# Optimization experiments

Measured on AMD Instinct MI355X. Metric: run time of the kernel, lower is better.

Reference implementation:

```python
import itertools
import jax, jax.numpy as jnp
import numpy as np

N_NODES = 100000
N_EDGES = 1600000
D = 32
C = 16
PDIM = 2  # pseudo-coordinate dim (SplineConv dim=E)


def setup_inputs() -> dict:
    key = jax.random.key(0)
    ks = jax.random.split(key, 16)
    s = 0.1
    inp = {
        "x": jax.random.normal(ks[0], (N_NODES, D), jnp.float32),
        "edge_index": jax.random.randint(ks[1], (2, N_EDGES), 0, N_NODES, jnp.int32),
        "edge_attr": jax.random.uniform(ks[2], (N_EDGES, PDIM), jnp.float32),
        # SplineConv 1: kernel_size=3 per dim -> K1 = 3**PDIM weight matrices
        "W1": jax.random.normal(ks[3], (3 ** PDIM, D, D), jnp.float32) * s,
        "root1": jax.random.normal(ks[4], (D, D), jnp.float32) * s,
        "bias1": jax.random.normal(ks[5], (D,), jnp.float32) * s,
        # SplineConv 2: kernel_size=5 per dim -> K2 = 5**PDIM weight matrices
        "W2": jax.random.normal(ks[6], (5 ** PDIM, D, D), jnp.float32) * s,
        "root2": jax.random.normal(ks[7], (D, D), jnp.float32) * s,
        "bias2": jax.random.normal(ks[8], (D,), jnp.float32) * s,
        "mlp1_w": jax.random.normal(ks[9], (D, D), jnp.float32) * s,
        "mlp1_b": jax.random.normal(ks[10], (D,), jnp.float32) * s,
        "mlp2_w": jax.random.normal(ks[11], (D, C), jnp.float32) * s,
        "mlp2_b": jax.random.normal(ks[12], (C,), jnp.float32) * s,
    }
    return inp


def _spline_conv(x, src, dst, pseudo, W, root, bias, ksize):
    """SplineConv, degree-1 open B-splines, aggr='mean' (torch_geometric default)."""
    N, d = x.shape
    dim = pseudo.shape[1]
    K = ksize ** dim
    E = src.shape[0]
    v = pseudo * (ksize - 1)          # [E, dim] in [0, ksize-1]
    bot = jnp.floor(v)
    frac = v - bot                    # linear B-spline fractional weight
    boti = bot.astype(jnp.int32)
    # Precompute per-kernel transformed features: y[n,k,:] = x[n] @ W[k]
    y = jnp.einsum('nd,kde->nke', x, W).reshape(N * K, d)
    msg = jnp.zeros((E, d), x.dtype)
    # (degree+1)^dim = 2^dim spline taps per edge; fixed small loop
    for offs in itertools.product((0, 1), repeat=dim):
        b = jnp.ones((E,), x.dtype)
        kidx = jnp.zeros((E,), jnp.int32)
        stride = 1
        for dd in range(dim):
            b = b * (frac[:, dd] if offs[dd] else (1.0 - frac[:, dd]))
            kidx = kidx + jnp.minimum(boti[:, dd] + offs[dd], ksize - 1) * stride
            stride *= ksize
        msg = msg + b[:, None] * y[src * K + kidx]
    agg = jax.ops.segment_sum(msg, dst, num_segments=N)
    cnt = jax.ops.segment_sum(jnp.ones((E,), x.dtype), dst, num_segments=N)
    cnt = jnp.clip(cnt, 1.0, None)
    return agg / cnt[:, None] + x @ root + bias


def reference(x, edge_index, edge_attr, W1, root1, bias1, W2, root2, bias2,
              mlp1_w, mlp1_b, mlp2_w, mlp2_b):
    src, dst = edge_index[0], edge_index[1]
    h = jax.nn.elu(_spline_conv(x, src, dst, edge_attr, W1, root1, bias1, 3))
    # dropout is identity at inference (F.dropout with training=False)
    h = jax.nn.elu(_spline_conv(h, src, dst, edge_attr, W2, root2, bias2, 5))
    h = jax.nn.relu(h @ mlp1_w + mlp1_b)
    h = jax.nn.relu(h @ mlp2_w + mlp2_b)
    return h
```

## Files before the change

kernel.cpp:

```cpp
#include <hip/hip_runtime.h>
#include <math.h>

#define NN 100000
#define NE 1600000
#define DD 32
#define CC 16
#define SCAN_B 391
#define NB (NE / 8)

typedef unsigned short bf16_t;
typedef __attribute__((ext_vector_type(8))) short short8v;
typedef __attribute__((ext_vector_type(4))) float float4v;

static inline unsigned gblocks(long total) { return (unsigned)((total + 255) / 256); }

__device__ inline bf16_t f2bf(float f) {
    unsigned u = __float_as_uint(f);
    u += 0x7fffu + ((u >> 16) & 1u);
    return (bf16_t)(u >> 16);
}
__device__ inline float bf2f(bf16_t h) { return __uint_as_float(((unsigned)h) << 16); }
__device__ inline unsigned pk2(float a, float b) {
    return (unsigned)f2bf(a) | ((unsigned)f2bf(b) << 16);
}

__global__ void zero_k(float* p, long n) {
    long i = (long)blockIdx.x * 256 + threadIdx.x;
    if (i < n) p[i] = 0.f;
}
__global__ void zero_int_k(int* p, int n) {
    int i = blockIdx.x * 256 + threadIdx.x;
    if (i < n) p[i] = 0;
}

__global__ void hist_k(const int* __restrict__ dst, int* __restrict__ cnt) {
    int e = blockIdx.x * 256 + threadIdx.x;
    if (e < NE) atomicAdd(&cnt[dst[e]], 1);
}
__global__ void s1_k(const int* __restrict__ cnt, int* __restrict__ offs,
                     int* __restrict__ bsum) {
    __shared__ int sm[256];
    int t = threadIdx.x, b = blockIdx.x;
    int g = b * 256 + t;
    int v = (g < NN) ? cnt[g] : 0;
    sm[t] = v;
    __syncthreads();
    for (int o = 1; o < 256; o <<= 1) {
        int u = (t >= o) ? sm[t - o] : 0;
        __syncthreads();
        sm[t] += u;
        __syncthreads();
    }
    if (g < NN) offs[g + 1] = sm[t];
    if (t == 255) bsum[b] = sm[255];
}
__global__ void s2_k(int* __restrict__ bsum) {
    __shared__ int sm[512];
    int t = threadIdx.x;
    int v = (t < SCAN_B) ? bsum[t] : 0;
    sm[t] = v;
    __syncthreads();
    for (int o = 1; o < 512; o <<= 1) {
        int u = (t >= o) ? sm[t - o] : 0;
        __syncthreads();
        sm[t] += u;
        __syncthreads();
    }
    if (t < SCAN_B) bsum[t] = sm[t] - v;
}
__global__ void s3_k(int* __restrict__ offs, const int* __restrict__ bsum) {
    int t = threadIdx.x, b = blockIdx.x;
    int g = b * 256 + t;
    if (g < NN) offs[g + 1] += bsum[b];
    if (g == 0) offs[0] = 0;
}
__global__ void copyoff_k(const int* __restrict__ offs, int* __restrict__ cur) {
    int g = blockIdx.x * 256 + threadIdx.x;
    if (g < NN) cur[g] = offs[g];
}

__global__ void fill_k(const int* __restrict__ dst, const int* __restrict__ src,
                       const float2* __restrict__ attr, int* __restrict__ cur,
                       uint2* __restrict__ emeta) {
    int e = blockIdx.x * 256 + threadIdx.x;
    if (e < NE) {
        int d = dst[e];
        int pos = atomicAdd(&cur[d], 1);
        float2 uv = attr[e];
        uint2 m;
        m.x = (unsigned)src[e];
        m.y = (unsigned)(uv.x * 65535.f + 0.5f) | ((unsigned)(uv.y * 65535.f + 0.5f) << 16);
        emeta[pos] = m;
    }
}

__global__ void dstbase_k(const int* __restrict__ offs, int* __restrict__ dstbase) {
    int b = blockIdx.x * 256 + threadIdx.x;
    if (b >= NB) return;
    int j = b * 8;
    int lo = 0, hi = NN - 1;
    while (lo < hi) {
        int mid = (lo + hi + 1) >> 1;
        if (offs[mid] <= j) lo = mid; else hi = mid - 1;
    }
    dstbase[b] = lo;
}

__global__ void castx_k(const float* __restrict__ in, bf16_t* __restrict__ outf) {
    int tid = blockIdx.x * 256 + threadIdx.x;
    if (tid >= NN * 4) return;
    int n = tid >> 2, q = tid & 3;
    const float4* ip = (const float4*)(in + (long)n * DD + q * 8);
    float4 v0 = ip[0], v1 = ip[1];
    int tile = n >> 4;
    int lane = (n & 15) + 16 * q;
    unsigned* op = (unsigned*)(outf + ((long)tile * 64 + lane) * 8);
    op[0] = pk2(v0.x, v0.y);
    op[1] = pk2(v0.z, v0.w);
    op[2] = pk2(v1.x, v1.y);
    op[3] = pk2(v1.z, v1.w);
}

__global__ void castw_k(const float* __restrict__ W, bf16_t* __restrict__ wtf, int K) {
    int tid = blockIdx.x * 256 + threadIdx.x;
    if (tid >= K * 2 * 64) return;
    int l = tid & 63;
    int half = (tid >> 6) & 1;
    int k = tid >> 7;
    int e = (l & 15) + 16 * half;
    int dbase = (l >> 4) * 8;
    bf16_t* op = wtf + (long)tid * 8;
#pragma unroll
    for (int r = 0; r < 8; ++r)
        op[r] = f2bf(W[(long)k * 1024 + (dbase + r) * DD + e]);
}

template<int K>
__global__ __launch_bounds__(64) void ymm_k(const short8v* __restrict__ xtf,
                                            const short8v* __restrict__ wtf,
                                            unsigned* __restrict__ y) {
    constexpr int RS = K * 16 + 4;
    __shared__ unsigned lds[16 * RS];
    const int l = threadIdx.x;
    const int tile = blockIdx.x;
    const int node = l & 15, g = l >> 4;

    short8v b = xtf[(long)tile * 64 + l];
    float4v zz = {0.f, 0.f, 0.f, 0.f};

    for (int k = 0; k < K; ++k) {
        float4v d0 = __builtin_amdgcn_mfma_f32_16x16x32_bf16(wtf[(2 * k + 0) * 64 + l], b, zz, 0, 0, 0);
        float4v d1 = __builtin_amdgcn_mfma_f32_16x16x32_bf16(wtf[(2 * k + 1) * 64 + l], b, zz, 0, 0, 0);
        unsigned* lr = &lds[node * RS + k * 16];
        lr[2 * g]     = pk2(d0[0], d0[1]);
        lr[2 * g + 1] = pk2(d0[2], d0[3]);
        lr[8 + 2 * g]     = pk2(d1[0], d1[1]);
        lr[8 + 2 * g + 1] = pk2(d1[2], d1[3]);
    }
    __syncthreads();

    unsigned* yb = y + (long)tile * (16 * K * 16);
    constexpr int TOT = 16 * K * 16;
    for (int off = l * 4; off < TOT; off += 256) {
        int nd = off / (K * 16);
        int rem = off - nd * (K * 16);
        const unsigned* lp = &lds[nd * RS + rem];
        uint4 v = make_uint4(lp[0], lp[1], lp[2], lp[3]);
        *(uint4*)(yb + off) = v;
    }
}

template<int KS>
__global__ __launch_bounds__(256) void edge_sr_k(
        const int* __restrict__ offs, const int* __restrict__ dstbase,
        const uint2* __restrict__ emeta, const bf16_t* __restrict__ y,
        float* __restrict__ agg) {
    constexpr int K = KS * KS;
    __shared__ float sm[8][33];
    __shared__ int sdst[8];
    const int tid = threadIdx.x;
    const int lane = tid & 31, g = tid >> 5;
    const int b = blockIdx.x;
    const int j = b * 8 + g;

    uint2 em = emeta[j];
    int n = dstbase[b];
    while (offs[n + 1] <= j) ++n;

    int s = (int)em.x;
    float u0 = (float)(em.y & 0xffffu) * (1.f / 65535.f);
    float u1 = (float)(em.y >> 16) * (1.f / 65535.f);
    float v0 = u0 * (KS - 1), v1 = u1 * (KS - 1);
    int i0 = min((int)v0, KS - 1), i1 = min((int)v1, KS - 1);
    float f0 = v0 - (float)i0, f1 = v1 - (float)i1;
    int q0 = min(i0 + 1, KS - 1), q1 = min(i1 + 1, KS - 1);
    const bf16_t* yb = y + (long)s * (K * DD) + lane;
    float y00 = bf2f(yb[(i0 + i1 * KS) * DD]);
    float y10 = bf2f(yb[(q0 + i1 * KS) * DD]);
    float y01 = bf2f(yb[(i0 + q1 * KS) * DD]);
    float y11 = bf2f(yb[(q0 + q1 * KS) * DD]);
    float m = (1.f - f0) * (1.f - f1) * y00 + f0 * (1.f - f1) * y10
            + (1.f - f0) * f1 * y01 + f0 * f1 * y11;

    sm[g][lane] = m;
    if (lane == 0) sdst[g] = n;
    __syncthreads();

    bool leader = (g == 0) || (sdst[g - 1] != n);
    if (leader) {
        float acc = sm[g][lane];
#pragma unroll
        for (int gg = 1; gg < 8; ++gg) {
            int g2 = g + gg;
            if (g2 >= 8 || sdst[g2] != n) break;
            acc += sm[g2][lane];
        }
        atomicAdd(&agg[(long)n * DD + lane], acc);
    }
}

__global__ __launch_bounds__(256) void fin1_k(
        const float* __restrict__ agg, const int* __restrict__ offs,
        const float* __restrict__ xin, const float* __restrict__ root,
        const float* __restrict__ bias, bf16_t* __restrict__ xtf) {
    const int lane = threadIdx.x & 31;
    const int grp = threadIdx.x >> 5;
    const int n = blockIdx.x * 8 + grp;
    if (n >= NN) return;
    int deg = offs[n + 1] - offs[n];
    float c = deg > 0 ? (float)deg : 1.f;
    float xv = xin[(long)n * DD + lane];
    float racc = 0.f;
#pragma unroll
    for (int d = 0; d < DD; ++d)
        racc = fmaf(__shfl(xv, d, 32), root[d * DD + lane], racc);
    float v = agg[(long)n * DD + lane] / c + racc + bias[lane];
    v = v > 0.f ? v : expm1f(v);
    xtf[((long)(n >> 4) * 64 + (n & 15) + 16 * (lane >> 3)) * 8 + (lane & 7)] = f2bf(v);
}

__global__ __launch_bounds__(256) void fin2_k(
        float* __restrict__ agg, const int* __restrict__ offs,
        const bf16_t* __restrict__ xtf, const float* __restrict__ root,
        const float* __restrict__ bias) {
    const int lane = threadIdx.x & 31;
    const int grp = threadIdx.x >> 5;
    const int n = blockIdx.x * 8 + grp;
    if (n >= NN) return;
    int deg = offs[n + 1] - offs[n];
    float c = deg > 0 ? (float)deg : 1.f;
    float xv = bf2f(xtf[((long)(n >> 4) * 64 + (n & 15) + 16 * (lane >> 3)) * 8 + (lane & 7)]);
    float racc = 0.f;
#pragma unroll
    for (int d = 0; d < DD; ++d)
        racc = fmaf(__shfl(xv, d, 32), root[d * DD + lane], racc);
    float v = agg[(long)n * DD + lane] / c + racc + bias[lane];
    agg[(long)n * DD + lane] = v > 0.f ? v : expm1f(v);
}

__global__ __launch_bounds__(256) void mlp_k(
        const float* __restrict__ h, const float* __restrict__ w1,
        const float* __restrict__ b1, const float* __restrict__ w2,
        const float* __restrict__ b2, float* __restrict__ out) {
    const int lane = threadIdx.x & 31;
    const int grp = threadIdx.x >> 5;
    const int n = blockIdx.x * 8 + grp;
    if (n >= NN) return;
    float hv = h[(long)n * DD + lane];
    float t = b1[lane];
#pragma unroll
    for (int d = 0; d < DD; ++d)
        t = fmaf(__shfl(hv, d, 32), w1[d * DD + lane], t);
    t = fmaxf(t, 0.f);
    int c = lane & (CC - 1);
    float o = 0.f;
#pragma unroll
    for (int d = 0; d < DD; ++d)
        o = fmaf(__shfl(t, d, 32), w2[d * CC + c], o);
    o += b2[c];
    o = fmaxf(o, 0.f);
    if (lane < CC) out[(long)n * CC + lane] = o;
}

extern "C" void kernel_launch(void* const* d_in, const int* in_sizes, int n_in,
                              void* d_out, int out_size, void* d_ws, size_t ws_size,
                              hipStream_t stream) {
    const float* x     = (const float*)d_in[0];
    const int*   ei    = (const int*)d_in[1];
    const float* attr  = (const float*)d_in[2];
    const float* W1    = (const float*)d_in[3];
    const float* root1 = (const float*)d_in[4];
    const float* bias1 = (const float*)d_in[5];
    const float* W2    = (const float*)d_in[6];
    const float* root2 = (const float*)d_in[7];
    const float* bias2 = (const float*)d_in[8];
    const float* m1w   = (const float*)d_in[9];
    const float* m1b   = (const float*)d_in[10];
    const float* m2w   = (const float*)d_in[11];
    const float* m2b   = (const float*)d_in[12];
    float* out = (float*)d_out;

    const int* srcp = ei;
    const int* dstp = ei + NE;

    int* offs = (int*)d_ws;
    int* dstbase = offs + NN + 8;
    uint2* emeta = (uint2*)(dstbase + NB);
    bf16_t* xtf = (bf16_t*)(emeta + NE);
    bf16_t* wtf1 = xtf + (size_t)NN * DD;
    bf16_t* wtf2 = wtf1 + 9 * 2 * 64 * 8;
    bf16_t* y = wtf2 + 25 * 2 * 64 * 8;
    float* agg = (float*)(y + (size_t)NN * 25 * DD);
    int* cur  = (int*)agg;
    int* bsum = (int*)agg + NN;

    const unsigned gn = (NN + 7) / 8;
    const unsigned gt = NN / 16;

    zero_int_k<<<gblocks(NN), 256, 0, stream>>>(cur, NN);
    hist_k<<<gblocks(NE), 256, 0, stream>>>(dstp, cur);
    s1_k<<<SCAN_B, 256, 0, stream>>>(cur, offs, bsum);
    s2_k<<<1, 512, 0, stream>>>(bsum);
    s3_k<<<SCAN_B, 256, 0, stream>>>(offs, bsum);
    copyoff_k<<<SCAN_B, 256, 0, stream>>>(offs, cur);
    fill_k<<<gblocks(NE), 256, 0, stream>>>(dstp, srcp, (const float2*)attr, cur, emeta);
    dstbase_k<<<gblocks(NB), 256, 0, stream>>>(offs, dstbase);

    castw_k<<<gblocks(9 * 2 * 64), 256, 0, stream>>>(W1, wtf1, 9);
    castw_k<<<gblocks(25 * 2 * 64), 256, 0, stream>>>(W2, wtf2, 25);

    castx_k<<<gblocks(NN * 4), 256, 0, stream>>>(x, xtf);
    ymm_k<9><<<gt, 64, 0, stream>>>((const short8v*)xtf, (const short8v*)wtf1, (unsigned*)y);
    zero_k<<<gblocks((long)NN * DD), 256, 0, stream>>>(agg, (long)NN * DD);
    edge_sr_k<3><<<NB, 256, 0, stream>>>(offs, dstbase, emeta, y, agg);
    fin1_k<<<gn, 256, 0, stream>>>(agg, offs, x, root1, bias1, xtf);

    ymm_k<25><<<gt, 64, 0, stream>>>((const short8v*)xtf, (const short8v*)wtf2, (unsigned*)y);
    zero_k<<<gblocks((long)NN * DD), 256, 0, stream>>>(agg, (long)NN * DD);
    edge_sr_k<5><<<NB, 256, 0, stream>>>(offs, dstbase, emeta, y, agg);
    fin2_k<<<gn, 256, 0, stream>>>(agg, offs, xtf, root2, bias2);

    mlp_k<<<gn, 256, 0, stream>>>(agg, m1w, m1b, m2w, m2b, out);
}
```

Baseline: 711.3 us.

## Interleave y layout for paired spline taps, drop LDS staging, fuse fin2 with MLP

The ymm kernel now writes packed bf16 pairs straight to global memory in an interleaved layout, with no LDS staging or barrier. In that layout, adjacent spline taps (i0 and i0+1) sit in consecutive 16-word chunks, so each edge's gather becomes two coalesced 32-bit loads per lane with a cross-half shuffle reduction. Clamping the base index to KS-2 keeps the B-spline result the same at the boundary. fin1 now zeroes agg in place, which removes the second zero kernel, and fin2 is fused with the MLP so the intermediate h2 no longer round-trips through memory. The risks are uncoalesced 8-byte scattered stores from ymm and extra shuffle work in the edge kernel.

New measurement: 670.4 us. 1.06x faster.

```diff
diff --git a/kernel.cpp b/kernel.cpp
--- a/kernel.cpp
+++ b/kernel.cpp
@@ -138,48 +138,37 @@
 template<int K>
 __global__ __launch_bounds__(64) void ymm_k(const short8v* __restrict__ xtf,
                                             const short8v* __restrict__ wtf,
-                                            unsigned* __restrict__ y) {
-    constexpr int RS = K * 16 + 4;
-    __shared__ unsigned lds[16 * RS];
+                                            uint2* __restrict__ y) {
     const int l = threadIdx.x;
     const int tile = blockIdx.x;
     const int node = l & 15, g = l >> 4;
 
     short8v b = xtf[(long)tile * 64 + l];
     float4v zz = {0.f, 0.f, 0.f, 0.f};
+    const long nb = ((long)tile * 16 + node) * K;
 
     for (int k = 0; k < K; ++k) {
         float4v d0 = __builtin_amdgcn_mfma_f32_16x16x32_bf16(wtf[(2 * k + 0) * 64 + l], b, zz, 0, 0, 0);
         float4v d1 = __builtin_amdgcn_mfma_f32_16x16x32_bf16(wtf[(2 * k + 1) * 64 + l], b, zz, 0, 0, 0);
-        unsigned* lr = &lds[node * RS + k * 16];
-        lr[2 * g]     = pk2(d0[0], d0[1]);
-        lr[2 * g + 1] = pk2(d0[2], d0[3]);
-        lr[8 + 2 * g]     = pk2(d1[0], d1[1]);
-        lr[8 + 2 * g + 1] = pk2(d1[2], d1[3]);
-    }
-    __syncthreads();
-
-    unsigned* yb = y + (long)tile * (16 * K * 16);
-    constexpr int TOT = 16 * K * 16;
-    for (int off = l * 4; off < TOT; off += 256) {
-        int nd = off / (K * 16);
-        int rem = off - nd * (K * 16);
-        const unsigned* lp = &lds[nd * RS + rem];
-        uint4 v = make_uint4(lp[0], lp[1], lp[2], lp[3]);
-        *(uint4*)(yb + off) = v;
+        uint2 s0, s1;
+        s0.x = pk2(d0[0], d0[1]); s0.y = pk2(d0[2], d0[3]);
+        s1.x = pk2(d1[0], d1[1]); s1.y = pk2(d1[2], d1[3]);
+        y[(nb + k) * 8 + g] = s0;
+        y[(nb + k) * 8 + 4 + g] = s1;
     }
 }
 
 template<int KS>
 __global__ __launch_bounds__(256) void edge_sr_k(
         const int* __restrict__ offs, const int* __restrict__ dstbase,
-        const uint2* __restrict__ emeta, const bf16_t* __restrict__ y,
+        const uint2* __restrict__ emeta, const unsigned* __restrict__ yu,
         float* __restrict__ agg) {
     constexpr int K = KS * KS;
-    __shared__ float sm[8][33];
+    __shared__ float smf[8][36];
     __shared__ int sdst[8];
     const int tid = threadIdx.x;
     const int lane = tid & 31, g = tid >> 5;
+    const int al = lane & 15, half = lane >> 4;
     const int b = blockIdx.x;
     const int j = b * 8 + g;
 
@@ -191,36 +180,41 @@
     float u0 = (float)(em.y & 0xffffu) * (1.f / 65535.f);
     float u1 = (float)(em.y >> 16) * (1.f / 65535.f);
     float v0 = u0 * (KS - 1), v1 = u1 * (KS - 1);
-    int i0 = min((int)v0, KS - 1), i1 = min((int)v1, KS - 1);
+    int i0 = min((int)v0, KS - 2), i1 = min((int)v1, KS - 2);
     float f0 = v0 - (float)i0, f1 = v1 - (float)i1;
-    int q0 = min(i0 + 1, KS - 1), q1 = min(i1 + 1, KS - 1);
-    const bf16_t* yb = y + (long)s * (K * DD) + lane;
-    float y00 = bf2f(yb[(i0 + i1 * KS) * DD]);
-    float y10 = bf2f(yb[(q0 + i1 * KS) * DD]);
-    float y01 = bf2f(yb[(i0 + q1 * KS) * DD]);
-    float y11 = bf2f(yb[(q0 + q1 * KS) * DD]);
-    float m = (1.f - f0) * (1.f - f1) * y00 + f0 * (1.f - f1) * y10
-            + (1.f - f0) * f1 * y01 + f0 * f1 * y11;
-
-    sm[g][lane] = m;
+
+    float wh = half ? f0 : (1.f - f0);
+    long base = ((long)s * K + i1 * KS + i0 + half) * 16 + al;
+    unsigned uA = yu[base];
+    unsigned uB = yu[base + KS * 16];
+    float wA = wh * (1.f - f1), wB = wh * f1;
+    float p0 = wA * bf2f((bf16_t)(uA & 0xffffu)) + wB * bf2f((bf16_t)(uB & 0xffffu));
+    float p1 = wA * bf2f((bf16_t)(uA >> 16)) + wB * bf2f((bf16_t)(uB >> 16));
+    p0 += __shfl_xor(p0, 16);
+    p1 += __shfl_xor(p1, 16);
+
+    if (half == 0) {
+        smf[g][2 * al] = p0;
+        smf[g][2 * al + 1] = p1;
+    }
     if (lane == 0) sdst[g] = n;
     __syncthreads();
 
     bool leader = (g == 0) || (sdst[g - 1] != n);
     if (leader) {
-        float acc = sm[g][lane];
+        float acc = smf[g][lane];
 #pragma unroll
         for (int gg = 1; gg < 8; ++gg) {
             int g2 = g + gg;
             if (g2 >= 8 || sdst[g2] != n) break;
-            acc += sm[g2][lane];
+            acc += smf[g2][lane];
         }
         atomicAdd(&agg[(long)n * DD + lane], acc);
     }
 }
 
 __global__ __launch_bounds__(256) void fin1_k(
-        const float* __restrict__ agg, const int* __restrict__ offs,
+        float* __restrict__ agg, const int* __restrict__ offs,
         const float* __restrict__ xin, const float* __restrict__ root,
         const float* __restrict__ bias, bf16_t* __restrict__ xtf) {
     const int lane = threadIdx.x & 31;
@@ -235,49 +229,41 @@
     for (int d = 0; d < DD; ++d)
         racc = fmaf(__shfl(xv, d, 32), root[d * DD + lane], racc);
     float v = agg[(long)n * DD + lane] / c + racc + bias[lane];
+    agg[(long)n * DD + lane] = 0.f;
     v = v > 0.f ? v : expm1f(v);
     xtf[((long)(n >> 4) * 64 + (n & 15) + 16 * (lane >> 3)) * 8 + (lane & 7)] = f2bf(v);
 }
 
-__global__ __launch_bounds__(256) void fin2_k(
-        float* __restrict__ agg, const int* __restrict__ offs,
+__global__ __launch_bounds__(256) void finmlp_k(
+        const float* __restrict__ agg, const int* __restrict__ offs,
         const bf16_t* __restrict__ xtf, const float* __restrict__ root,
-        const float* __restrict__ bias) {
+        const float* __restrict__ bias, const float* __restrict__ w1,
+        const float* __restrict__ b1, const float* __restrict__ w2,
+        const float* __restrict__ b2, float* __restrict__ out) {
     const int lane = threadIdx.x & 31;
     const int grp = threadIdx.x >> 5;
     const int n = blockIdx.x * 8 + grp;
     if (n >= NN) return;
     int deg = offs[n + 1] - offs[n];
     float c = deg > 0 ? (float)deg : 1.f;
-    float xv = bf2f(xtf[((long)(n >> 4) * 64 + (n & 15) + 16 * (lane >> 3)) * 8 + (lane & 7)]);
+    float h1 = bf2f(xtf[((long)(n >> 4) * 64 + (n & 15) + 16 * (lane >> 3)) * 8 + (lane & 7)]);
     float racc = 0.f;
 #pragma unroll
     for (int d = 0; d < DD; ++d)
-        racc = fmaf(__shfl(xv, d, 32), root[d * DD + lane], racc);
-    float v = agg[(long)n * DD + lane] / c + racc + bias[lane];
-    agg[(long)n * DD + lane] = v > 0.f ? v : expm1f(v);
-}
-
-__global__ __launch_bounds__(256) void mlp_k(
-        const float* __restrict__ h, const float* __restrict__ w1,
-        const float* __restrict__ b1, const float* __restrict__ w2,
-        const float* __restrict__ b2, float* __restrict__ out) {
-    const int lane = threadIdx.x & 31;
-    const int grp = threadIdx.x >> 5;
-    const int n = blockIdx.x * 8 + grp;
-    if (n >= NN) return;
-    float hv = h[(long)n * DD + lane];
+        racc = fmaf(__shfl(h1, d, 32), root[d * DD + lane], racc);
+    float h2 = agg[(long)n * DD + lane] / c + racc + bias[lane];
+    h2 = h2 > 0.f ? h2 : expm1f(h2);
     float t = b1[lane];
 #pragma unroll
     for (int d = 0; d < DD; ++d)
-        t = fmaf(__shfl(hv, d, 32), w1[d * DD + lane], t);
+        t = fmaf(__shfl(h2, d, 32), w1[d * DD + lane], t);
     t = fmaxf(t, 0.f);
-    int c = lane & (CC - 1);
+    int cc = lane & (CC - 1);
     float o = 0.f;
 #pragma unroll
     for (int d = 0; d < DD; ++d)
-        o = fmaf(__shfl(t, d, 32), w2[d * CC + c], o);
-    o += b2[c];
+        o = fmaf(__shfl(t, d, 32), w2[d * CC + cc], o);
+    o += b2[cc];
     o = fmaxf(o, 0.f);
     if (lane < CC) out[(long)n * CC + lane] = o;
 }
@@ -330,15 +316,14 @@
     castw_k<<<gblocks(25 * 2 * 64), 256, 0, stream>>>(W2, wtf2, 25);
 
     castx_k<<<gblocks(NN * 4), 256, 0, stream>>>(x, xtf);
-    ymm_k<9><<<gt, 64, 0, stream>>>((const short8v*)xtf, (const short8v*)wtf1, (unsigned*)y);
+    ymm_k<9><<<gt, 64, 0, stream>>>((const short8v*)xtf, (const short8v*)wtf1, (uint2*)y);
     zero_k<<<gblocks((long)NN * DD), 256, 0, stream>>>(agg, (long)NN * DD);
-    edge_sr_k<3><<<NB, 256, 0, stream>>>(offs, dstbase, emeta, y, agg);
+    edge_sr_k<3><<<NB, 256, 0, stream>>>(offs, dstbase, emeta, (const unsigned*)y, agg);
     fin1_k<<<gn, 256, 0, stream>>>(agg, offs, x, root1, bias1, xtf);
 
-    ymm_k<25><<<gt, 64, 0, stream>>>((const short8v*)xtf, (const short8v*)wtf2, (unsigned*)y);
-    zero_k<<<gblocks((long)NN * DD), 256, 0, stream>>>(agg, (long)NN * DD);
-    edge_sr_k<5><<<NB, 256, 0, stream>>>(offs, dstbase, emeta, y, agg);
-    fin2_k<<<gn, 256, 0, stream>>>(agg, offs, xtf, root2, bias2);
-
-    mlp_k<<<gn, 256, 0, stream>>>(agg, m1w, m1b, m2w, m2b, out);
-}
+    ymm_k<25><<<gt, 64, 0, stream>>>((const short8v*)xtf, (const short8v*)wtf2, (uint2*)y);
+    edge_sr_k<5><<<NB, 256, 0, stream>>>(offs, dstbase, emeta, (const unsigned*)y, agg);
+
+    finmlp_k<<<gn, 256, 0, stream>>>(agg, offs, xtf, root2, bias2,
+                                     m1w, m1b, m2w, m2b, out);
+}
```
